# Kernel tuning notes

Measured on AMD Instinct MI355X. Metric: run time of the kernel, lower is better.

The kernel has to match this reference:

```python
import jax, jax.numpy as jnp
import numpy as np

B, N, DEG = 32, 1024, 8
E = B * N * DEG
NT = B * N
F_IN, HID, EDIM, NR, HD = 64, 128, 16, 16, 4
NEG = 0.2  # leaky_relu negative slope (alpha)
K1 = int(np.ceil(0.8 * N))    # 820 kept nodes per graph after pool1
K2 = int(np.ceil(0.8 * K1))   # 656 kept nodes per graph after pool2


def setup_inputs() -> dict:
    key = jax.random.key(0)
    ks = jax.random.split(key, 20)
    nrm = lambda i, shp, s=0.05: jax.random.normal(ks[i], shp, jnp.float32) * s
    x = jax.random.normal(ks[0], (NT, F_IN), jnp.float32)
    off = (jnp.arange(B) * N)[:, None]
    src = (jax.random.randint(ks[1], (B, N * DEG), 0, N) + off).reshape(-1)
    dst = (jax.random.randint(ks[2], (B, N * DEG), 0, N) + off).reshape(-1)
    edge_index = jnp.stack([src, dst]).astype(jnp.int32)
    edge_attr = jax.random.normal(ks[3], (E, EDIM), jnp.float32)
    action = jax.random.normal(ks[4], (B, NR), jnp.float32)
    return dict(
        x=x, edge_attr=edge_attr, action=action,
        W1l=nrm(5, (F_IN, HD * HID)), b1l=jnp.zeros(HD * HID),
        W1r=nrm(6, (F_IN, HD * HID)), b1r=jnp.zeros(HD * HID),
        W1e=nrm(7, (EDIM, HD * HID)), att1=nrm(8, (HD, HID)), bias1=jnp.zeros(HID),
        W2l=nrm(9, (HID, HD * HID)), b2l=jnp.zeros(HD * HID),
        W2r=nrm(10, (HID, HD * HID)), b2r=jnp.zeros(HD * HID),
        W2e=nrm(11, (EDIM, HD * HID)), att2=nrm(12, (HD, HID)), bias2=jnp.zeros(HID),
        p1=nrm(13, (HID,), 0.1), p2=nrm(14, (HID,), 0.1),
        Wf1=nrm(15, (2 * HID + NR, HID)), bf1=jnp.zeros(HID),
        Wf2=nrm(16, (HID, HID)), bf2=jnp.zeros(HID),
        Wf3=nrm(17, (HID, 1), 0.003), bf3=jnp.zeros(1),
        edge_index=edge_index,
    )


def _gatv2(x, edge_index, edge_attr, edge_mask, Wl, bl, Wr, br, We, att, bias):
    # PyG GATv2Conv, concat=False (mean over heads), eval mode (no dropout).
    src, dst = edge_index[0], edge_index[1]
    n = x.shape[0]
    xl = (x @ Wl + bl).reshape(n, HD, HID)   # source transform (x_j)
    xr = (x @ Wr + br).reshape(n, HD, HID)   # target transform (x_i)
    ef = (edge_attr @ We).reshape(-1, HD, HID)
    m = jax.nn.leaky_relu(xl[src] + xr[dst] + ef, NEG)          # [E,H,C]
    logits = jnp.where(edge_mask[:, None], (m * att).sum(-1), -1e9)  # [E,H]
    mx = jax.ops.segment_max(logits, dst, num_segments=n)
    a = jnp.exp(logits - mx[dst])
    den = jax.ops.segment_sum(a, dst, num_segments=n)
    alpha = (a / (den[dst] + 1e-16)) * edge_mask[:, None]       # softmax per dst, masked edges zeroed
    out = jax.ops.segment_sum(xl[src] * alpha[..., None], dst, num_segments=n)
    return out.mean(axis=1) + bias


def _topk(x, node_mask, p, k):
    # PyG TopKPooling: score = x@p/||p||, gate = tanh(score), keep top-k per graph.
    score = (x @ p) / (jnp.linalg.norm(p) + 1e-16)
    gate = jnp.tanh(score)
    s = jnp.where(node_mask, score, -jnp.inf).reshape(B, N)
    idx = jax.lax.top_k(s, k)[1]                                # [B,k]
    keep = jnp.zeros((B, N), bool).at[jnp.arange(B)[:, None], idx].set(True).reshape(-1)
    return x * gate[:, None], keep


def reference(x, edge_attr, action, W1l, b1l, W1r, b1r, W1e, att1, bias1,
              W2l, b2l, W2r, b2r, W2e, att2, bias2, p1, p2,
              Wf1, bf1, Wf2, bf2, Wf3, bf3, edge_index):
    src, dst = edge_index[0], edge_index[1]
    em0 = jnp.ones((E,), bool)
    h = jax.nn.relu(_gatv2(x, edge_index, edge_attr, em0,
                           W1l, b1l, W1r, b1r, W1e, att1, bias1))
    h, keep1 = _topk(h, jnp.ones((NT,), bool), p1, K1)
    em1 = keep1[src] & keep1[dst]
    h = jax.nn.relu(_gatv2(h, edge_index, edge_attr, em1,
                           W2l, b2l, W2r, b2r, W2e, att2, bias2))
    h, keep2 = _topk(h, keep1, p2, K2)
    hb = h.reshape(B, N, HID)
    mb = keep2.reshape(B, N)[..., None]
    gmx = jnp.where(mb, hb, -jnp.inf).max(axis=1)               # global max pool over kept nodes
    gav = (hb * mb).sum(axis=1) / K2                            # global mean pool (K2 kept per graph)
    z = jnp.concatenate([gmx, gav, action], axis=1)             # [B, 2*HID+NR]
    z = jax.nn.relu(z @ Wf1 + bf1)
    z = jax.nn.relu(z @ Wf2 + bf2)
    return z @ Wf3 + bf3
```

## Files before the change

kernel.cpp:

```cpp
#include <hip/hip_runtime.h>
#include <math.h>

#define NTN 32768
#define NBG 32
#define NN  1024
#define EPG 8192
#define EE  262144
#define FIN 64
#define HIDC 128
#define HD  4
#define HC  512
#define EDIM 16
#define NR  16
#define KP1 820
#define KP2 656
#define NKEPT (KP1 * NBG)
#define NEGS 0.2f
#define NPB 2
#define SHIFT 10.0f

template<int K>
__global__ __launch_bounds__(256) void gemm_node3(const float* __restrict__ A,
                                                  const float* __restrict__ Wl,
                                                  const float* __restrict__ bl,
                                                  const float* __restrict__ Wr,
                                                  const float* __restrict__ br,
                                                  const float* __restrict__ gs,
                                                  const int* __restrict__ ids,
                                                  float* __restrict__ Cl,
                                                  float* __restrict__ Cr,
                                                  const int* __restrict__ perm,
                                                  const float* __restrict__ ea,
                                                  float* __restrict__ eaP) {
    __shared__ float a_s[64][K];
    __shared__ int rid_s[64];
    __shared__ float g_s[64];
    int t = threadIdx.x;
    int rb = blockIdx.x >> 2, cg = blockIdx.x & 3;
    int row0 = rb * 64;
    if (t < 64) {
        int rid = ids ? ids[row0 + t] : (row0 + t);
        rid_s[t] = rid;
        g_s[t] = gs ? tanhf(gs[rid]) : 1.0f;
    }
    __syncthreads();
    for (int i = t; i < 64 * K; i += 256) {
        int r = i / K, k = i % K;
        a_s[r][k] = A[(size_t)rid_s[r] * K + k] * g_s[r];
    }
    __syncthreads();
    int tc = cg * 128 + (t & 63) * 2;
    int rg = (t >> 6) * 16;
    float accl0[16], accl1[16], accr0[16], accr1[16];
    float2 blv = *(const float2*)&bl[tc];
    float2 brv = *(const float2*)&br[tc];
    #pragma unroll
    for (int r = 0; r < 16; r++) { accl0[r] = blv.x; accl1[r] = blv.y; accr0[r] = brv.x; accr1[r] = brv.y; }
    for (int k = 0; k < K; k++) {
        float2 wl = *(const float2*)&Wl[(size_t)k * HC + tc];
        float2 wr = *(const float2*)&Wr[(size_t)k * HC + tc];
        #pragma unroll
        for (int r = 0; r < 16; r++) {
            float a = a_s[rg + r][k];
            accl0[r] += a * wl.x; accl1[r] += a * wl.y;
            accr0[r] += a * wr.x; accr1[r] += a * wr.y;
        }
    }
    for (int r = 0; r < 16; r++) {
        size_t base = (size_t)rid_s[rg + r] * HC + tc;
        *(float2*)&Cl[base] = make_float2(accl0[r], accl1[r]);
        *(float2*)&Cr[base] = make_float2(accr0[r], accr1[r]);
    }
    if (perm) {
        int ng = gridDim.x * 256;
        for (int p = blockIdx.x * 256 + t; p < EE; p += ng) {
            int e = perm[p];
            const float4* s4 = (const float4*)(ea + (size_t)e * EDIM);
            float4* d4 = (float4*)(eaP + (size_t)p * EDIM);
            d4[0] = s4[0]; d4[1] = s4[1]; d4[2] = s4[2]; d4[3] = s4[3];
        }
    }
}

__global__ __launch_bounds__(1024) void csr_build(const int* __restrict__ dst,
                                                  const int* __restrict__ src,
                                                  int* __restrict__ off,
                                                  int* __restrict__ esrc,
                                                  int* __restrict__ perm,
                                                  const float* __restrict__ p1,
                                                  const float* __restrict__ p2,
                                                  float* __restrict__ pn) {
    int g = blockIdx.x, t = threadIdx.x;
    __shared__ int degS[NN];
    __shared__ int scanS[NN];
    __shared__ int curS[NN];
    degS[t] = 0;
    __syncthreads();
    int eb = g * EPG;
    #pragma unroll
    for (int i = t; i < EPG; i += 1024) atomicAdd(&degS[dst[eb + i] - g * NN], 1);
    __syncthreads();
    int dg = degS[t];
    scanS[t] = dg;
    for (int o = 1; o < NN; o <<= 1) {
        __syncthreads();
        int v = (t >= o) ? scanS[t - o] : 0;
        __syncthreads();
        scanS[t] += v;
    }
    __syncthreads();
    int excl = scanS[t] - dg;
    off[g * NN + t] = eb + excl;
    curS[t] = excl;
    if (g == NBG - 1 && t == NN - 1) off[NTN] = EE;
    if (g == 0 && t < 64) {
        float a = p1[t] * p1[t] + p1[t + 64] * p1[t + 64];
        float b = p2[t] * p2[t] + p2[t + 64] * p2[t + 64];
        #pragma unroll
        for (int sft = 32; sft; sft >>= 1) { a += __shfl_xor(a, sft, 64); b += __shfl_xor(b, sft, 64); }
        if (t == 0) { pn[0] = 1.f / (sqrtf(a) + 1e-16f); pn[1] = 1.f / (sqrtf(b) + 1e-16f); }
    }
    __syncthreads();
    #pragma unroll
    for (int i = t; i < EPG; i += 1024) {
        int e = eb + i;
        int ld = dst[e] - g * NN;
        int p = eb + atomicAdd(&curS[ld], 1);
        esrc[p] = src[e];
        perm[p] = e;
    }
}

template<bool L2>
__global__ __launch_bounds__(256, 4) void gat_dst(
        const float* __restrict__ xl, const float* __restrict__ xr,
        const float* __restrict__ eaP, const float* __restrict__ We,
        const float* __restrict__ att, const float* __restrict__ bias,
        const float* __restrict__ pvec, const float* __restrict__ pnInv,
        const int* __restrict__ esrc, const int* __restrict__ off,
        const int* __restrict__ keep,
        float* __restrict__ out, float* __restrict__ score, int nblk) {
    int bid = blockIdx.x;
    int swz = (bid & 7) * (nblk >> 3) + (bid >> 3);
    int d0 = swz * NPB;
    int t = threadIdx.x;
    int w = t >> 6, lane = t & 63;
    int c = w * HIDC + lane * 2;
    __shared__ float red[NPB][HC];
    __shared__ float red2[NPB][HIDC];
    float we0[EDIM], we1[EDIM];
    #pragma unroll
    for (int k = 0; k < EDIM; k++) {
        we0[k] = We[k * HC + c];
        we1[k] = We[k * HC + c + 1];
    }
    float at0 = att[c], at1 = att[c + 1];

    for (int n = 0; n < NPB; n++) {
        int d = d0 + n;
        float denA = 0.f, aA0 = 0.f, aA1 = 0.f;
        float denB = 0.f, aB0 = 0.f, aB1 = 0.f;
        bool live = !L2 || (keep[d] != 0);
        if (live) {
            float2 xrv = *(const float2*)&xr[((size_t)d << 9) + c];
            int e0 = off[d], e1 = off[d + 1];
            int ei = e0;
            for (; ei + 4 <= e1; ei += 4) {
                int s[4]; float mk[4]; float2 xv[4]; float p[4];
                #pragma unroll
                for (int j = 0; j < 4; j++) {
                    int sv = esrc[ei + j];
                    if (L2) {
                        mk[j] = sv >= 0 ? 1.f : 0.f;
                        s[j] = sv >= 0 ? sv : 0;
                    } else {
                        s[j] = sv;
                    }
                }
                #pragma unroll
                for (int j = 0; j < 4; j++) xv[j] = *(const float2*)&xl[((size_t)s[j] << 9) + c];
                #pragma unroll
                for (int j = 0; j < 4; j++) {
                    const float4* eap = (const float4*)(eaP + ((size_t)(ei + j) << 4));
                    float4 E0 = eap[0], E1 = eap[1], E2 = eap[2], E3 = eap[3];
                    float ev[16] = {E0.x, E0.y, E0.z, E0.w, E1.x, E1.y, E1.z, E1.w,
                                    E2.x, E2.y, E2.z, E2.w, E3.x, E3.y, E3.z, E3.w};
                    float ef0 = 0.f, ef1 = 0.f;
                    #pragma unroll
                    for (int k = 0; k < EDIM; k++) { ef0 += ev[k] * we0[k]; ef1 += ev[k] * we1[k]; }
                    float v0 = xv[j].x + xrv.x + ef0; v0 = v0 > 0.f ? v0 : NEGS * v0;
                    float v1 = xv[j].y + xrv.y + ef1; v1 = v1 > 0.f ? v1 : NEGS * v1;
                    p[j] = v0 * at0 + v1 * at1;
                }
                #pragma unroll
                for (int sft = 32; sft; sft >>= 1) {
                    #pragma unroll
                    for (int j = 0; j < 4; j++) p[j] += __shfl_xor(p[j], sft, 64);
                }
                float w0 = __expf(p[0] - SHIFT);
                float w1 = __expf(p[1] - SHIFT);
                float w2 = __expf(p[2] - SHIFT);
                float w3 = __expf(p[3] - SHIFT);
                if (L2) { w0 *= mk[0]; w1 *= mk[1]; w2 *= mk[2]; w3 *= mk[3]; }
                denA += w0; aA0 += w0 * xv[0].x; aA1 += w0 * xv[0].y;
                denB += w1; aB0 += w1 * xv[1].x; aB1 += w1 * xv[1].y;
                denA += w2; aA0 += w2 * xv[2].x; aA1 += w2 * xv[2].y;
                denB += w3; aB0 += w3 * xv[3].x; aB1 += w3 * xv[3].y;
            }
            for (; ei < e1; ei++) {
                int sv = esrc[ei];
                float mk = 1.f;
                int s = sv;
                if (L2) { mk = sv >= 0 ? 1.f : 0.f; s = sv >= 0 ? sv : 0; }
                const float4* eap = (const float4*)(eaP + ((size_t)ei << 4));
                float4 E0 = eap[0], E1 = eap[1], E2 = eap[2], E3 = eap[3];
                float2 xv = *(const float2*)&xl[((size_t)s << 9) + c];
                float ev[16] = {E0.x, E0.y, E0.z, E0.w, E1.x, E1.y, E1.z, E1.w,
                                E2.x, E2.y, E2.z, E2.w, E3.x, E3.y, E3.z, E3.w};
                float ef0 = 0.f, ef1 = 0.f;
                #pragma unroll
                for (int k = 0; k < EDIM; k++) { ef0 += ev[k] * we0[k]; ef1 += ev[k] * we1[k]; }
                float v0 = xv.x + xrv.x + ef0; v0 = v0 > 0.f ? v0 : NEGS * v0;
                float v1 = xv.y + xrv.y + ef1; v1 = v1 > 0.f ? v1 : NEGS * v1;
                float p = v0 * at0 + v1 * at1;
                #pragma unroll
                for (int sft = 32; sft; sft >>= 1) p += __shfl_xor(p, sft, 64);
                float wt = __expf(p - SHIFT);
                if (L2) wt *= mk;
                denA += wt; aA0 += wt * xv.x; aA1 += wt * xv.y;
            }
        }
        float inv = 1.f / (denA + denB + 1e-16f);
        red[n][c] = (aA0 + aB0) * inv;
        red[n][c + 1] = (aA1 + aB1) * inv;
    }
    __syncthreads();
    {
        int n2 = t >> 7, tc = t & 127;
        float v = (red[n2][tc] + red[n2][tc + 128] + red[n2][tc + 256] + red[n2][tc + 384]) * 0.25f
                  + bias[tc];
        v = fmaxf(v, 0.f);
        out[((size_t)(d0 + n2) << 7) + tc] = v;
        red2[n2][tc] = v * pvec[tc];
    }
    __syncthreads();
    if (t < 128) {
        int n3 = t >> 6, l2 = t & 63;
        float sv = red2[n3][l2] + red2[n3][l2 + 64];
        #pragma unroll
        for (int sft = 32; sft; sft >>= 1) sv += __shfl_xor(sv, sft, 64);
        if (l2 == 0) score[d0 + n3] = sv * pnInv[0];
    }
}

__global__ __launch_bounds__(512) void topk_sel(const float* __restrict__ score,
                                                const int* __restrict__ mask, int k,
                                                int* __restrict__ keep, int* __restrict__ klist,
                                                const int* __restrict__ esrc,
                                                int* __restrict__ esrc2) {
    __shared__ float v[NN];
    __shared__ short id[NN];
    __shared__ char kpS[NN];
    int g = blockIdx.x, t = threadIdx.x;
    for (int i = t; i < NN; i += 512) {
        int n = g * NN + i;
        bool mk = mask ? (mask[n] != 0) : true;
        v[i] = mk ? score[n] : -INFINITY;
        id[i] = (short)i;
    }
    __syncthreads();
    for (int kk = 2; kk <= NN; kk <<= 1) {
        for (int j = kk >> 1; j > 0; j >>= 1) {
            #pragma unroll 2
            for (int i = t; i < NN; i += 512) {
                int ixj = i ^ j;
                if (ixj > i) {
                    bool up = ((i & kk) == 0);
                    float a = v[i], b2 = v[ixj];
                    short ia = id[i], ib = id[ixj];
                    bool aFirst = (a > b2) || (a == b2 && ia < ib);
                    if (up ? !aFirst : aFirst) { v[i] = b2; v[ixj] = a; id[i] = ib; id[ixj] = ia; }
                }
            }
            __syncthreads();
        }
    }
    for (int i = t; i < NN; i += 512) {
        int kp = (i < k) ? 1 : 0;
        keep[g * NN + id[i]] = kp;
        kpS[id[i]] = (char)kp;
        if (klist && kp) klist[g * k + i] = g * NN + id[i];
    }
    __syncthreads();
    if (esrc2) {
        int eb = g * EPG;
        for (int i = t; i < EPG; i += 512) {
            int sv = esrc[eb + i];
            esrc2[eb + i] = kpS[sv - g * NN] ? sv : -1;
        }
    }
}

__global__ __launch_bounds__(512) void tail(const float* __restrict__ score,
                                            const int* __restrict__ mask,
                                            const float* __restrict__ h,
                                            const float* __restrict__ action,
                                            const float* __restrict__ Wf1, const float* __restrict__ bf1,
                                            const float* __restrict__ Wf2, const float* __restrict__ bf2,
                                            const float* __restrict__ Wf3, const float* __restrict__ bf3,
                                            float* __restrict__ out) {
    int g = blockIdx.x, t = threadIdx.x;
    __shared__ float v[NN];
    __shared__ short id[NN];
    __shared__ float gt_s[NN];
    __shared__ char kp_s[NN];
    __shared__ float smx[4][HIDC], ssm[4][HIDC];
    __shared__ float zs[2 * HIDC + NR], z1[HIDC], z2[HIDC], rr[HIDC];
    for (int i = t; i < NN; i += 512) {
        int n = g * NN + i;
        bool mk = (mask[n] != 0);
        v[i] = mk ? score[n] : -INFINITY;
        id[i] = (short)i;
        kp_s[i] = 0;
        gt_s[i] = 0.f;
    }
    __syncthreads();
    for (int kk = 2; kk <= NN; kk <<= 1) {
        for (int j = kk >> 1; j > 0; j >>= 1) {
            #pragma unroll 2
            for (int i = t; i < NN; i += 512) {
                int ixj = i ^ j;
                if (ixj > i) {
                    bool up = ((i & kk) == 0);
                    float a = v[i], b2 = v[ixj];
                    short ia = id[i], ib = id[ixj];
                    bool aFirst = (a > b2) || (a == b2 && ia < ib);
                    if (up ? !aFirst : aFirst) { v[i] = b2; v[ixj] = a; id[i] = ib; id[ixj] = ia; }
                }
            }
            __syncthreads();
        }
    }
    for (int i = t; i < NN; i += 512) {
        if (i < KP2) {
            int nid = id[i];
            kp_s[nid] = 1;
            gt_s[nid] = tanhf(score[g * NN + nid]);
        }
    }
    __syncthreads();
    int c = t & 127, ch = t >> 7;
    float mx = -INFINITY, sm = 0.f;
    for (int n = ch * 256; n < ch * 256 + 256; n++) {
        if (kp_s[n]) {
            float hv = h[(size_t)(g * NN + n) * HIDC + c] * gt_s[n];
            mx = fmaxf(mx, hv);
            sm += hv;
        }
    }
    smx[ch][c] = mx; ssm[ch][c] = sm;
    __syncthreads();
    if (t < HIDC) {
        mx = fmaxf(fmaxf(smx[0][t], smx[1][t]), fmaxf(smx[2][t], smx[3][t]));
        sm = ssm[0][t] + ssm[1][t] + ssm[2][t] + ssm[3][t];
        zs[t] = mx;
        zs[HIDC + t] = sm / (float)KP2;
        if (t < NR) zs[2 * HIDC + t] = action[g * NR + t];
    }
    __syncthreads();
    if (t < HIDC) {
        float a = bf1[t];
        for (int k = 0; k < 2 * HIDC + NR; k++) a += zs[k] * Wf1[(size_t)k * HIDC + t];
        z1[t] = fmaxf(a, 0.f);
    }
    __syncthreads();
    if (t < HIDC) {
        float a = bf2[t];
        for (int k = 0; k < HIDC; k++) a += z1[k] * Wf2[(size_t)k * HIDC + t];
        z2[t] = fmaxf(a, 0.f);
        rr[t] = z2[t] * Wf3[t];
    }
    __syncthreads();
    for (int s = 64; s; s >>= 1) {
        if (t < s) rr[t] += rr[t + s];
        __syncthreads();
    }
    if (t == 0) out[g] = rr[0] + bf3[0];
}

extern "C" void kernel_launch(void* const* d_in, const int* in_sizes, int n_in,
                              void* d_out, int out_size, void* d_ws, size_t ws_size,
                              hipStream_t stream) {
    const float* x    = (const float*)d_in[0];
    const float* ea   = (const float*)d_in[1];
    const float* act  = (const float*)d_in[2];
    const float* W1l  = (const float*)d_in[3];
    const float* b1l  = (const float*)d_in[4];
    const float* W1r  = (const float*)d_in[5];
    const float* b1r  = (const float*)d_in[6];
    const float* W1e  = (const float*)d_in[7];
    const float* att1 = (const float*)d_in[8];
    const float* bias1= (const float*)d_in[9];
    const float* W2l  = (const float*)d_in[10];
    const float* b2l  = (const float*)d_in[11];
    const float* W2r  = (const float*)d_in[12];
    const float* b2r  = (const float*)d_in[13];
    const float* W2e  = (const float*)d_in[14];
    const float* att2 = (const float*)d_in[15];
    const float* bias2= (const float*)d_in[16];
    const float* p1   = (const float*)d_in[17];
    const float* p2   = (const float*)d_in[18];
    const float* Wf1  = (const float*)d_in[19];
    const float* bf1  = (const float*)d_in[20];
    const float* Wf2  = (const float*)d_in[21];
    const float* bf2  = (const float*)d_in[22];
    const float* Wf3  = (const float*)d_in[23];
    const float* bf3  = (const float*)d_in[24];
    const int*   eix  = (const int*)d_in[25];
    const int* srcA = eix;
    const int* dstA = eix + EE;

    float* ws    = (float*)d_ws;
    float* xl    = ws;
    float* xr    = xl + (size_t)NTN * HC;
    float* h     = xr + (size_t)NTN * HC;
    float* score1= h + (size_t)NTN * HIDC;
    float* score2= score1 + NTN;
    float* pn    = score2 + NTN;
    int* keep1 = (int*)(pn + 2);
    int* klist = keep1 + NTN;
    int* off   = klist + NKEPT;
    int* esrc  = off + NTN + 1;
    int* esrc2 = esrc + EE;
    int* perm  = esrc2 + EE;
    float* eaP = (float*)(perm + EE);

    csr_build<<<NBG, 1024, 0, stream>>>(dstA, srcA, off, esrc, perm, p1, p2, pn);

    gemm_node3<FIN><<<(NTN / 64) * 4, 256, 0, stream>>>(x, W1l, b1l, W1r, b1r, nullptr, nullptr,
                                                        xl, xr, perm, ea, eaP);
    gat_dst<false><<<NTN / NPB, 256, 0, stream>>>(xl, xr, eaP, W1e, att1, bias1, p1, pn, esrc, off,
                                                  nullptr, h, score1, NTN / NPB);

    topk_sel<<<NBG, 512, 0, stream>>>(score1, nullptr, KP1, keep1, klist, esrc, esrc2);

    gemm_node3<HIDC><<<(NKEPT / 64) * 4, 256, 0, stream>>>(h, W2l, b2l, W2r, b2r, score1, klist,
                                                           xl, xr, nullptr, nullptr, nullptr);
    gat_dst<true><<<NTN / NPB, 256, 0, stream>>>(xl, xr, eaP, W2e, att2, bias2, p2, pn + 1, esrc2, off,
                                                 keep1, h, score2, NTN / NPB);

    tail<<<NBG, 512, 0, stream>>>(score2, keep1, h, act,
                                  Wf1, bf1, Wf2, bf2, Wf3, bf3, (float*)d_out);
}
```

Baseline: 530.9 us.

## Fold CSR build into layer-1 GEMM launch and split edge-attr permute kernel

The standalone 32-block CSR build kernel is merged into the layer-1 node GEMM as extra blocks, so the CSR construction runs at the same time as the GEMM instead of before it. Each CSR block now uses 256 threads and scans four nodes per thread. The edge-attribute permutation, which previously ran after the GEMM inside the same kernel, moves to its own fully parallel kernel with one float4 per thread. CSR offsets in the GAT kernel are also loaded through readfirstlane so they are treated as scalars. The trade-off is one extra launch and CSR blocks that now have fewer threads each.

```diff
diff --git a/kernel.cpp b/kernel.cpp
--- a/kernel.cpp
+++ b/kernel.cpp
@@ -19,7 +19,7 @@
 #define NPB 2
 #define SHIFT 10.0f
 
-template<int K>
+template<int K, bool WITHCSR>
 __global__ __launch_bounds__(256) void gemm_node3(const float* __restrict__ A,
                                                   const float* __restrict__ Wl,
                                                   const float* __restrict__ bl,
@@ -29,13 +29,65 @@
                                                   const int* __restrict__ ids,
                                                   float* __restrict__ Cl,
                                                   float* __restrict__ Cr,
-                                                  const int* __restrict__ perm,
-                                                  const float* __restrict__ ea,
-                                                  float* __restrict__ eaP) {
+                                                  int ngemm,
+                                                  const int* __restrict__ dst,
+                                                  const int* __restrict__ src,
+                                                  int* __restrict__ off,
+                                                  int* __restrict__ esrc,
+                                                  int* __restrict__ perm,
+                                                  const float* __restrict__ p1,
+                                                  const float* __restrict__ p2,
+                                                  float* __restrict__ pn) {
     __shared__ float a_s[64][K];
     __shared__ int rid_s[64];
     __shared__ float g_s[64];
     int t = threadIdx.x;
+    if (WITHCSR && blockIdx.x >= ngemm) {
+        int g = blockIdx.x - ngemm;
+        int* degS  = (int*)a_s;
+        int* scanS = degS + NN;
+        int* curS  = scanS + 256;
+        for (int i = t; i < NN; i += 256) degS[i] = 0;
+        __syncthreads();
+        int eb = g * EPG;
+        for (int i = t; i < EPG; i += 256) atomicAdd(&degS[dst[eb + i] - g * NN], 1);
+        __syncthreads();
+        int l[4]; int sum = 0;
+        #pragma unroll
+        for (int j = 0; j < 4; j++) { l[j] = degS[t * 4 + j]; sum += l[j]; }
+        scanS[t] = sum;
+        for (int o = 1; o < 256; o <<= 1) {
+            __syncthreads();
+            int v = (t >= o) ? scanS[t - o] : 0;
+            __syncthreads();
+            scanS[t] += v;
+        }
+        __syncthreads();
+        int run = scanS[t] - sum;
+        #pragma unroll
+        for (int j = 0; j < 4; j++) {
+            off[g * NN + t * 4 + j] = eb + run;
+            curS[t * 4 + j] = run;
+            run += l[j];
+        }
+        if (g == NBG - 1 && t == 255) off[NTN] = EE;
+        if (g == 0 && t < 64) {
+            float a = p1[t] * p1[t] + p1[t + 64] * p1[t + 64];
+            float b = p2[t] * p2[t] + p2[t + 64] * p2[t + 64];
+            #pragma unroll
+            for (int sft = 32; sft; sft >>= 1) { a += __shfl_xor(a, sft, 64); b += __shfl_xor(b, sft, 64); }
+            if (t == 0) { pn[0] = 1.f / (sqrtf(a) + 1e-16f); pn[1] = 1.f / (sqrtf(b) + 1e-16f); }
+        }
+        __syncthreads();
+        for (int i = t; i < EPG; i += 256) {
+            int e = eb + i;
+            int ld = dst[e] - g * NN;
+            int p = eb + atomicAdd(&curS[ld], 1);
+            esrc[p] = src[e];
+            perm[p] = e;
+        }
+        return;
+    }
     int rb = blockIdx.x >> 2, cg = blockIdx.x & 3;
     int row0 = rb * 64;
     if (t < 64) {
@@ -71,64 +123,13 @@
         *(float2*)&Cl[base] = make_float2(accl0[r], accl1[r]);
         *(float2*)&Cr[base] = make_float2(accr0[r], accr1[r]);
     }
-    if (perm) {
-        int ng = gridDim.x * 256;
-        for (int p = blockIdx.x * 256 + t; p < EE; p += ng) {
-            int e = perm[p];
-            const float4* s4 = (const float4*)(ea + (size_t)e * EDIM);
-            float4* d4 = (float4*)(eaP + (size_t)p * EDIM);
-            d4[0] = s4[0]; d4[1] = s4[1]; d4[2] = s4[2]; d4[3] = s4[3];
-        }
-    }
-}
-
-__global__ __launch_bounds__(1024) void csr_build(const int* __restrict__ dst,
-                                                  const int* __restrict__ src,
-                                                  int* __restrict__ off,
-                                                  int* __restrict__ esrc,
-                                                  int* __restrict__ perm,
-                                                  const float* __restrict__ p1,
-                                                  const float* __restrict__ p2,
-                                                  float* __restrict__ pn) {
-    int g = blockIdx.x, t = threadIdx.x;
-    __shared__ int degS[NN];
-    __shared__ int scanS[NN];
-    __shared__ int curS[NN];
-    degS[t] = 0;
-    __syncthreads();
-    int eb = g * EPG;
-    #pragma unroll
-    for (int i = t; i < EPG; i += 1024) atomicAdd(&degS[dst[eb + i] - g * NN], 1);
-    __syncthreads();
-    int dg = degS[t];
-    scanS[t] = dg;
-    for (int o = 1; o < NN; o <<= 1) {
-        __syncthreads();
-        int v = (t >= o) ? scanS[t - o] : 0;
-        __syncthreads();
-        scanS[t] += v;
-    }
-    __syncthreads();
-    int excl = scanS[t] - dg;
-    off[g * NN + t] = eb + excl;
-    curS[t] = excl;
-    if (g == NBG - 1 && t == NN - 1) off[NTN] = EE;
-    if (g == 0 && t < 64) {
-        float a = p1[t] * p1[t] + p1[t + 64] * p1[t + 64];
-        float b = p2[t] * p2[t] + p2[t + 64] * p2[t + 64];
-        #pragma unroll
-        for (int sft = 32; sft; sft >>= 1) { a += __shfl_xor(a, sft, 64); b += __shfl_xor(b, sft, 64); }
-        if (t == 0) { pn[0] = 1.f / (sqrtf(a) + 1e-16f); pn[1] = 1.f / (sqrtf(b) + 1e-16f); }
-    }
-    __syncthreads();
-    #pragma unroll
-    for (int i = t; i < EPG; i += 1024) {
-        int e = eb + i;
-        int ld = dst[e] - g * NN;
-        int p = eb + atomicAdd(&curS[ld], 1);
-        esrc[p] = src[e];
-        perm[p] = e;
-    }
+}
+
+__global__ void ea_permute(const int* __restrict__ perm, const float* __restrict__ ea,
+                           float* __restrict__ eaP) {
+    int id = blockIdx.x * 256 + threadIdx.x;
+    int p = id >> 2, q = id & 3;
+    ((float4*)eaP)[p * 4 + q] = ((const float4*)ea)[perm[p] * 4 + q];
 }
 
 template<bool L2>
@@ -163,7 +164,8 @@
         bool live = !L2 || (keep[d] != 0);
         if (live) {
             float2 xrv = *(const float2*)&xr[((size_t)d << 9) + c];
-            int e0 = off[d], e1 = off[d + 1];
+            int e0 = __builtin_amdgcn_readfirstlane(off[d]);
+            int e1 = __builtin_amdgcn_readfirstlane(off[d + 1]);
             int ei = e0;
             for (; ei + 4 <= e1; ei += 4) {
                 int s[4]; float mk[4]; float2 xv[4]; float p[4];
@@ -435,17 +437,21 @@
     int* perm  = esrc2 + EE;
     float* eaP = (float*)(perm + EE);
 
-    csr_build<<<NBG, 1024, 0, stream>>>(dstA, srcA, off, esrc, perm, p1, p2, pn);
-
-    gemm_node3<FIN><<<(NTN / 64) * 4, 256, 0, stream>>>(x, W1l, b1l, W1r, b1r, nullptr, nullptr,
-                                                        xl, xr, perm, ea, eaP);
+    const int NG1 = (NTN / 64) * 4;
+
+    gemm_node3<FIN, true><<<NG1 + NBG, 256, 0, stream>>>(x, W1l, b1l, W1r, b1r, nullptr, nullptr,
+                                                         xl, xr, NG1,
+                                                         dstA, srcA, off, esrc, perm, p1, p2, pn);
+    ea_permute<<<EE * 4 / 256, 256, 0, stream>>>(perm, ea, eaP);
     gat_dst<false><<<NTN / NPB, 256, 0, stream>>>(xl, xr, eaP, W1e, att1, bias1, p1, pn, esrc, off,
                                                   nullptr, h, score1, NTN / NPB);
 
     topk_sel<<<NBG, 512, 0, stream>>>(score1, nullptr, KP1, keep1, klist, esrc, esrc2);
 
-    gemm_node3<HIDC><<<(NKEPT / 64) * 4, 256, 0, stream>>>(h, W2l, b2l, W2r, b2r, score1, klist,
-                                                           xl, xr, nullptr, nullptr, nullptr);
+    gemm_node3<HIDC, false><<<(NKEPT / 64) * 4, 256, 0, stream>>>(h, W2l, b2l, W2r, b2r, score1, klist,
+                                                                  xl, xr, 0,
+                                                                  nullptr, nullptr, nullptr, nullptr,
+                                                                  nullptr, nullptr, nullptr, nullptr);
     gat_dst<true><<<NTN / NPB, 256, 0, stream>>>(xl, xr, eaP, W2e, att2, bias2, p2, pn + 1, esrc2, off,
                                                  keep1, h, score2, NTN / NPB);
 
```

New measurement: 547.6 us. 3.1% more time.

## Split each wavefront into two half-waves processing edge pairs with float4 channels

Applied to the files above, without the earlier changes.

The GAT aggregation kernel now has each 64-lane wavefront split into two 32-lane halves. Each half handles a different edge, and each lane covers four channels with float4 loads. This cuts the cross-lane reduction from six shuffle steps to five per edge and widens the gathers. The edge-feature weights are no longer held in registers but reloaded from global/L1 per edge, trading register pressure for extra loads. The node GEMM also unrolls the K loop by four and reads A values as float4 from shared memory.

```diff
diff --git a/kernel.cpp b/kernel.cpp
--- a/kernel.cpp
+++ b/kernel.cpp
@@ -56,14 +56,20 @@
     float2 brv = *(const float2*)&br[tc];
     #pragma unroll
     for (int r = 0; r < 16; r++) { accl0[r] = blv.x; accl1[r] = blv.y; accr0[r] = brv.x; accr1[r] = brv.y; }
-    for (int k = 0; k < K; k++) {
-        float2 wl = *(const float2*)&Wl[(size_t)k * HC + tc];
-        float2 wr = *(const float2*)&Wr[(size_t)k * HC + tc];
+    for (int k = 0; k < K; k += 4) {
+        float2 wl[4], wr[4];
+        #pragma unroll
+        for (int kk = 0; kk < 4; kk++) {
+            wl[kk] = *(const float2*)&Wl[(size_t)(k + kk) * HC + tc];
+            wr[kk] = *(const float2*)&Wr[(size_t)(k + kk) * HC + tc];
+        }
         #pragma unroll
         for (int r = 0; r < 16; r++) {
-            float a = a_s[rg + r][k];
-            accl0[r] += a * wl.x; accl1[r] += a * wl.y;
-            accr0[r] += a * wr.x; accr1[r] += a * wr.y;
+            float4 a4 = *(const float4*)&a_s[rg + r][k];
+            accl0[r] += a4.x * wl[0].x + a4.y * wl[1].x + a4.z * wl[2].x + a4.w * wl[3].x;
+            accl1[r] += a4.x * wl[0].y + a4.y * wl[1].y + a4.z * wl[2].y + a4.w * wl[3].y;
+            accr0[r] += a4.x * wr[0].x + a4.y * wr[1].x + a4.z * wr[2].x + a4.w * wr[3].x;
+            accr1[r] += a4.x * wr[0].y + a4.y * wr[1].y + a4.z * wr[2].y + a4.w * wr[3].y;
         }
     }
     for (int r = 0; r < 16; r++) {
@@ -145,95 +151,77 @@
     int d0 = swz * NPB;
     int t = threadIdx.x;
     int w = t >> 6, lane = t & 63;
-    int c = w * HIDC + lane * 2;
+    int half = lane >> 5, l32 = lane & 31;
+    int cb = w * HIDC + l32 * 4;
     __shared__ float red[NPB][HC];
     __shared__ float red2[NPB][HIDC];
-    float we0[EDIM], we1[EDIM];
-    #pragma unroll
-    for (int k = 0; k < EDIM; k++) {
-        we0[k] = We[k * HC + c];
-        we1[k] = We[k * HC + c + 1];
-    }
-    float at0 = att[c], at1 = att[c + 1];
+    float4 at4 = *(const float4*)&att[cb];
+
+#define PAIR(EI, MASKED)                                                            \
+    {                                                                               \
+        int eidx = (EI) + half;                                                     \
+        bool valid = !MASKED || (eidx < e1);                                        \
+        int ec = valid ? eidx : (e1 - 1);                                           \
+        int sv = esrc[ec];                                                          \
+        float mk = valid ? 1.f : 0.f;                                               \
+        int s = sv;                                                                 \
+        if (L2) { if (sv < 0) { mk = 0.f; s = 0; } }                                \
+        float4 xv = *(const float4*)&xl[((size_t)s << 9) + cb];                     \
+        const float4* eap = (const float4*)(eaP + ((size_t)ec << 4));               \
+        float4 E0 = eap[0], E1 = eap[1], E2 = eap[2], E3 = eap[3];                  \
+        float ev[16] = {E0.x, E0.y, E0.z, E0.w, E1.x, E1.y, E1.z, E1.w,             \
+                        E2.x, E2.y, E2.z, E2.w, E3.x, E3.y, E3.z, E3.w};            \
+        float4 ef = make_float4(0.f, 0.f, 0.f, 0.f);                                \
+        _Pragma("unroll")                                                           \
+        for (int k = 0; k < EDIM; k++) {                                            \
+            float4 wv = *(const float4*)&We[k * HC + cb];                           \
+            ef.x += ev[k] * wv.x; ef.y += ev[k] * wv.y;                             \
+            ef.z += ev[k] * wv.z; ef.w += ev[k] * wv.w;                             \
+        }                                                                           \
+        float v0 = xv.x + xr4.x + ef.x; v0 = v0 > 0.f ? v0 : NEGS * v0;             \
+        float v1 = xv.y + xr4.y + ef.y; v1 = v1 > 0.f ? v1 : NEGS * v1;             \
+        float v2 = xv.z + xr4.z + ef.z; v2 = v2 > 0.f ? v2 : NEGS * v2;             \
+        float v3 = xv.w + xr4.w + ef.w; v3 = v3 > 0.f ? v3 : NEGS * v3;             \
+        float p = v0 * at4.x + v1 * at4.y + v2 * at4.z + v3 * at4.w;                \
+        p += __shfl_xor(p, 1, 64);                                                  \
+        p += __shfl_xor(p, 2, 64);                                                  \
+        p += __shfl_xor(p, 4, 64);                                                  \
+        p += __shfl_xor(p, 8, 64);                                                  \
+        p += __shfl_xor(p, 16, 64);                                                 \
+        float wt = mk * __expf(p - SHIFT);                                          \
+        den += wt;                                                                  \
+        acc.x += wt * xv.x; acc.y += wt * xv.y;                                     \
+        acc.z += wt * xv.z; acc.w += wt * xv.w;                                     \
+    }
 
     for (int n = 0; n < NPB; n++) {
         int d = d0 + n;
-        float denA = 0.f, aA0 = 0.f, aA1 = 0.f;
-        float denB = 0.f, aB0 = 0.f, aB1 = 0.f;
-        bool live = !L2 || (keep[d] != 0);
-        if (live) {
-            float2 xrv = *(const float2*)&xr[((size_t)d << 9) + c];
+        float4 acc = make_float4(0.f, 0.f, 0.f, 0.f);
+        float den = 0.f;
+        bool livedst = !L2 || (keep[d] != 0);
+        if (livedst) {
+            float4 xr4 = *(const float4*)&xr[((size_t)d << 9) + cb];
             int e0 = off[d], e1 = off[d + 1];
             int ei = e0;
             for (; ei + 4 <= e1; ei += 4) {
-                int s[4]; float mk[4]; float2 xv[4]; float p[4];
-                #pragma unroll
-                for (int j = 0; j < 4; j++) {
-                    int sv = esrc[ei + j];
-                    if (L2) {
-                        mk[j] = sv >= 0 ? 1.f : 0.f;
-                        s[j] = sv >= 0 ? sv : 0;
-                    } else {
-                        s[j] = sv;
-                    }
-                }
-                #pragma unroll
-                for (int j = 0; j < 4; j++) xv[j] = *(const float2*)&xl[((size_t)s[j] << 9) + c];
-                #pragma unroll
-                for (int j = 0; j < 4; j++) {
-                    const float4* eap = (const float4*)(eaP + ((size_t)(ei + j) << 4));
-                    float4 E0 = eap[0], E1 = eap[1], E2 = eap[2], E3 = eap[3];
-                    float ev[16] = {E0.x, E0.y, E0.z, E0.w, E1.x, E1.y, E1.z, E1.w,
-                                    E2.x, E2.y, E2.z, E2.w, E3.x, E3.y, E3.z, E3.w};
-                    float ef0 = 0.f, ef1 = 0.f;
-                    #pragma unroll
-                    for (int k = 0; k < EDIM; k++) { ef0 += ev[k] * we0[k]; ef1 += ev[k] * we1[k]; }
-                    float v0 = xv[j].x + xrv.x + ef0; v0 = v0 > 0.f ? v0 : NEGS * v0;
-                    float v1 = xv[j].y + xrv.y + ef1; v1 = v1 > 0.f ? v1 : NEGS * v1;
-                    p[j] = v0 * at0 + v1 * at1;
-                }
-                #pragma unroll
-                for (int sft = 32; sft; sft >>= 1) {
-                    #pragma unroll
-                    for (int j = 0; j < 4; j++) p[j] += __shfl_xor(p[j], sft, 64);
-                }
-                float w0 = __expf(p[0] - SHIFT);
-                float w1 = __expf(p[1] - SHIFT);
-                float w2 = __expf(p[2] - SHIFT);
-                float w3 = __expf(p[3] - SHIFT);
-                if (L2) { w0 *= mk[0]; w1 *= mk[1]; w2 *= mk[2]; w3 *= mk[3]; }
-                denA += w0; aA0 += w0 * xv[0].x; aA1 += w0 * xv[0].y;
-                denB += w1; aB0 += w1 * xv[1].x; aB1 += w1 * xv[1].y;
-                denA += w2; aA0 += w2 * xv[2].x; aA1 += w2 * xv[2].y;
-                denB += w3; aB0 += w3 * xv[3].x; aB1 += w3 * xv[3].y;
+                PAIR(ei, false);
+                PAIR(ei + 2, false);
             }
-            for (; ei < e1; ei++) {
-                int sv = esrc[ei];
-                float mk = 1.f;
-                int s = sv;
-                if (L2) { mk = sv >= 0 ? 1.f : 0.f; s = sv >= 0 ? sv : 0; }
-                const float4* eap = (const float4*)(eaP + ((size_t)ei << 4));
-                float4 E0 = eap[0], E1 = eap[1], E2 = eap[2], E3 = eap[3];
-                float2 xv = *(const float2*)&xl[((size_t)s << 9) + c];
-                float ev[16] = {E0.x, E0.y, E0.z, E0.w, E1.x, E1.y, E1.z, E1.w,
-                                E2.x, E2.y, E2.z, E2.w, E3.x, E3.y, E3.z, E3.w};
-                float ef0 = 0.f, ef1 = 0.f;
-                #pragma unroll
-                for (int k = 0; k < EDIM; k++) { ef0 += ev[k] * we0[k]; ef1 += ev[k] * we1[k]; }
-                float v0 = xv.x + xrv.x + ef0; v0 = v0 > 0.f ? v0 : NEGS * v0;
-                float v1 = xv.y + xrv.y + ef1; v1 = v1 > 0.f ? v1 : NEGS * v1;
-                float p = v0 * at0 + v1 * at1;
-                #pragma unroll
-                for (int sft = 32; sft; sft >>= 1) p += __shfl_xor(p, sft, 64);
-                float wt = __expf(p - SHIFT);
-                if (L2) wt *= mk;
-                denA += wt; aA0 += wt * xv.x; aA1 += wt * xv.y;
+            for (; ei < e1; ei += 2) {
+                PAIR(ei, true);
             }
         }
-        float inv = 1.f / (denA + denB + 1e-16f);
-        red[n][c] = (aA0 + aB0) * inv;
-        red[n][c + 1] = (aA1 + aB1) * inv;
-    }
+        den += __shfl_xor(den, 32, 64);
+        acc.x += __shfl_xor(acc.x, 32, 64);
+        acc.y += __shfl_xor(acc.y, 32, 64);
+        acc.z += __shfl_xor(acc.z, 32, 64);
+        acc.w += __shfl_xor(acc.w, 32, 64);
+        float inv = 1.f / (den + 1e-16f);
+        if (half == 0) {
+            *(float4*)&red[n][cb] = make_float4(acc.x * inv, acc.y * inv, acc.z * inv, acc.w * inv);
+        }
+    }
+#undef PAIR
     __syncthreads();
     {
         int n2 = t >> 7, tc = t & 127;
```

New measurement: 1.134 ms. 2.14x slower.
